# Kernel optimization log

Hardware: AMD Instinct MI355X
Metric: run time of the kernel (lower is better)

Reference implementation:

```python
import jax, jax.numpy as jnp
import numpy as np

B, T, D, H = 512, 512, 128, 64


def _lstm(x, Wih, Whh, b):
    """Single-layer batch-first LSTM, PyTorch gate order (i, f, g, o).
    x: [B, T, Din]; Wih: [4Hc, Din]; Whh: [4Hc, Hc]; b: [4Hc] (= b_ih + b_hh).
    Returns (outputs [B, T, Hc], final_hidden [B, Hc]).
    """
    Hc = Whh.shape[1]
    Bn = x.shape[0]
    # Precompute input projections for all timesteps: [B, T, 4Hc]
    xp = jnp.einsum('bti,gi->btg', x, Wih) + b

    def step(carry, xt):
        h, c = carry
        g = xt + h @ Whh.T                      # [B, 4Hc]
        i = jax.nn.sigmoid(g[:, :Hc])
        f = jax.nn.sigmoid(g[:, Hc:2 * Hc])
        gg = jnp.tanh(g[:, 2 * Hc:3 * Hc])
        o = jax.nn.sigmoid(g[:, 3 * Hc:])
        c = f * c + i * gg
        h = o * jnp.tanh(c)
        return (h, c), h

    init = (jnp.zeros((Bn, Hc), x.dtype), jnp.zeros((Bn, Hc), x.dtype))
    (h_last, _), ys = jax.lax.scan(step, init, jnp.swapaxes(xp, 0, 1))
    return jnp.swapaxes(ys, 0, 1), h_last


def setup_inputs() -> dict:
    key = jax.random.key(0)
    ks = jax.random.split(key, 7)
    se = 1.0 / np.sqrt(H)   # PyTorch LSTM init scale (encoder, hidden=H)
    sd = 1.0 / np.sqrt(D)   # decoder, hidden=D
    return {
        'x': jax.random.normal(ks[0], (B, T, D), jnp.float32),
        'Wih_e': jax.random.uniform(ks[1], (4 * H, D), jnp.float32, -se, se),
        'Whh_e': jax.random.uniform(ks[2], (4 * H, H), jnp.float32, -se, se),
        'b_e': jax.random.uniform(ks[3], (4 * H,), jnp.float32, -se, se),
        'Wih_d': jax.random.uniform(ks[4], (4 * D, H), jnp.float32, -sd, sd),
        'Whh_d': jax.random.uniform(ks[5], (4 * D, D), jnp.float32, -sd, sd),
        'b_d': jax.random.uniform(ks[6], (4 * D,), jnp.float32, -sd, sd),
    }


def reference(x, Wih_e, Whh_e, b_e, Wih_d, Whh_d, b_d):
    # Encoder: take final hidden state [B, H]
    _, h = _lstm(x, Wih_e, Whh_e, b_e)
    # hidden.repeat(T,1,1).permute(1,0,2) -> tile across time: [B, T, H]
    hrep = jnp.broadcast_to(h[:, None, :], (h.shape[0], x.shape[1], h.shape[1]))
    # Decoder: full output sequence [B, T, D]
    reconstructed, _ = _lstm(hrep, Wih_d, Whh_d, b_d)
    return reconstructed
```

## Files before the change

### kernel.cpp

```cpp
#include <hip/hip_runtime.h>

#define TT 512

typedef float f32x2 __attribute__((ext_vector_type(2)));
typedef float f32x4 __attribute__((ext_vector_type(4)));

template<int CTRL>
__device__ __forceinline__ float dpp_mov(float v) {
    return __int_as_float(__builtin_amdgcn_mov_dpp(__float_as_int(v), CTRL, 0xF, 0xF, true));
}
__device__ __forceinline__ float swz_xor4(float v) {
    return __int_as_float(__builtin_amdgcn_ds_swizzle(__float_as_int(v), 0x101F));
}
__device__ __forceinline__ void pk(f32x2& a, f32x2 w, f32x2 v) {
    asm("v_pk_fma_f32 %0, %1, %2, %0" : "+v"(a) : "v"(w), "v"(v));
}

__device__ __forceinline__ float merge8(float* s) {
    s[0] += dpp_mov<0xB1>(s[4]);
    s[1] += dpp_mov<0xB1>(s[5]);
    s[2] += dpp_mov<0xB1>(s[6]);
    s[3] += dpp_mov<0xB1>(s[7]);
    s[0] += dpp_mov<0x4E>(s[2]);
    s[1] += dpp_mov<0x4E>(s[3]);
    return s[0] + swz_xor4(s[1]);
}

__global__ __launch_bounds__(1024, 4)
void dec_kernel(const float* __restrict__ h_enc,
                const float* __restrict__ Wih,
                const float* __restrict__ Whh,
                const float* __restrict__ bias,
                float* __restrict__ out)
{
    const int tid = threadIdx.x;
    const int gg  = tid >> 3;
    const int q   = tid & 7;
    const int q0 = q & 1, q1 = (q >> 1) & 1, q2 = (q >> 2) & 1;
    const int msk2 = (q0 << 1) | q1;
    const int b0  = blockIdx.x * 2;

    __shared__ __align__(16) float he[2][64];
    __shared__ __align__(16) float hb[2][2 * 160];

    if (tid < 128) he[tid >> 6][tid & 63] = h_enc[(size_t)(b0 + (tid >> 6)) * 64 + (tid & 63)];
    if (tid < 256) {
        int r = tid >> 7, j = tid & 127;
        hb[0][r * 160 + j + 4 * (j >> 4)] = 0.f;
    }

    f32x4 w[4][4];
    #pragma unroll
    for (int m = 0; m < 4; ++m) {
        const float* src = Whh + (size_t)((m ^ msk2) * 128 + gg) * 128 + 16 * q;
        #pragma unroll
        for (int c = 0; c < 4; ++c) w[m][c] = *(const f32x4*)(src + 4 * c);
    }

    const int t4own = 2 * q0 + q1;
    const float sA = (t4own == 2) ? 2.f : 1.f;
    const float sC = (t4own == 2) ? -1.f : 0.f;
    const bool writer = (q0 == 0) && (q1 == 0);
    const int rr  = q2;
    const int oA  = q2 * 160;
    const int oB  = (q2 ^ 1) * 160;
    const int kres = 20 * q;
    const int pwj = q2 * 160 + gg + 4 * (gg >> 4);

    __syncthreads();

    float xp;
    {
        const float* heA = he[q2] + 8 * q;
        const float* heB = he[q2 ^ 1] + 8 * q;
        f32x4 hA0 = *(const f32x4*)heA, hA1 = *(const f32x4*)(heA + 4);
        f32x4 hB0 = *(const f32x4*)heB, hB1 = *(const f32x4*)(heB + 4);
        float s[8];
        #pragma unroll
        for (int m = 0; m < 4; ++m) {
            const float* ws = Wih + (size_t)((m ^ msk2) * 128 + gg) * 64 + 8 * q;
            f32x4 w0 = *(const f32x4*)ws, w1 = *(const f32x4*)(ws + 4);
            f32x2 aA = {0.f, 0.f}, aB = {0.f, 0.f};
            pk(aA, w0.lo, hA0.lo); pk(aA, w0.hi, hA0.hi);
            pk(aA, w1.lo, hA1.lo); pk(aA, w1.hi, hA1.hi);
            pk(aB, w0.lo, hB0.lo); pk(aB, w0.hi, hB0.hi);
            pk(aB, w1.lo, hB1.lo); pk(aB, w1.hi, hB1.hi);
            s[2 * m]     = aA.x + aA.y;
            s[2 * m + 1] = aB.x + aB.y;
        }
        xp = merge8(s) + bias[t4own * 128 + gg];
    }

    float c_state = 0.f;
    size_t optr = ((size_t)(b0 + rr) * TT) * 128 + gg;

#define DSTEP(CUR, NXT) {                                                      \
    const float* bAp = (CUR) + oA + kres;                                      \
    const float* bBp = (CUR) + oB + kres;                                      \
    f32x4 ch[4]; f32x2 accA[4], accB[4];                                       \
    _Pragma("unroll") for (int c = 0; c < 4; ++c) ch[c] = *(const f32x4*)(bAp + 4 * c); \
    _Pragma("unroll") for (int m = 0; m < 4; ++m) { f32x2 z2 = {0.f, 0.f};     \
        _Pragma("unroll") for (int c = 0; c < 4; ++c) { pk(z2, w[m][c].lo, ch[c].lo); pk(z2, w[m][c].hi, ch[c].hi); } \
        accA[m] = z2; }                                                        \
    _Pragma("unroll") for (int c = 0; c < 4; ++c) ch[c] = *(const f32x4*)(bBp + 4 * c); \
    _Pragma("unroll") for (int m = 0; m < 4; ++m) { f32x2 z2 = {0.f, 0.f};     \
        _Pragma("unroll") for (int c = 0; c < 4; ++c) { pk(z2, w[m][c].lo, ch[c].lo); pk(z2, w[m][c].hi, ch[c].hi); } \
        accB[m] = z2; }                                                        \
    float s[8];                                                                \
    _Pragma("unroll") for (int m = 0; m < 4; ++m) {                            \
        s[2 * m] = accA[m].x + accA[m].y; s[2 * m + 1] = accB[m].x + accB[m].y; } \
    float z = merge8(s) + xp;                                                  \
    float ez = __expf(-z * sA);                                                \
    float v  = fmaf(__builtin_amdgcn_rcpf(1.0f + ez), sA, sC);                 \
    float vi = dpp_mov<0x00>(v); float vg = dpp_mov<0x55>(v);                  \
    float vf = dpp_mov<0xAA>(v); float vo = dpp_mov<0xFF>(v);                  \
    c_state = fmaf(vf, c_state, vi * vg);                                      \
    float e2 = __expf(-2.f * c_state);                                         \
    float hv = vo * fmaf(__builtin_amdgcn_rcpf(1.f + e2), 2.f, -1.f);          \
    if (writer) { (NXT)[pwj] = hv; out[optr] = hv; }                           \
    optr += 128;                                                               \
    __syncthreads(); }

    #pragma unroll 1
    for (int t = 0; t < TT; t += 2) {
        DSTEP(hb[0], hb[1]);
        DSTEP(hb[1], hb[0]);
    }
#undef DSTEP
}

__global__ __launch_bounds__(512, 2)
void enc_kernel(const float* __restrict__ x,
                const float* __restrict__ Wih,
                const float* __restrict__ Whh,
                const float* __restrict__ bias,
                float* __restrict__ h_out)
{
    const int tid = threadIdx.x;
    const int gg  = tid >> 3;
    const int q   = tid & 7;
    const int q0 = q & 1, q1 = (q >> 1) & 1, q2 = (q >> 2) & 1;
    const int msk2 = (q0 << 1) | q1;
    const int b0  = blockIdx.x * 2;

    __shared__ __align__(16) float xh[2][2 * 224];

    f32x4 w[4][6];
    #pragma unroll
    for (int m = 0; m < 4; ++m) {
        int row = (m ^ msk2) * 64 + gg;
        #pragma unroll
        for (int c = 0; c < 6; ++c) {
            int k0 = 24 * q + 4 * c;
            const float* src = (k0 < 128) ? (Wih + (size_t)row * 128 + k0)
                                          : (Whh + (size_t)row * 64 + (k0 - 128));
            w[m][c] = *(const f32x4*)src;
        }
    }

    const int t4own = 2 * q0 + q1;
    const float sA = (t4own == 2) ? 2.f : 1.f;
    const float sC = (t4own == 2) ? -1.f : 0.f;
    const bool writer = (q0 == 0) && (q1 == 0);
    const int rr  = q2;
    const int oA  = q2 * 224;
    const int oB  = (q2 ^ 1) * 224;
    const int kres = 28 * q;
    const int hj  = 128 + gg;
    const int pwj = q2 * 224 + hj + 4 * (hj / 24);
    const float xpc = bias[t4own * 64 + gg];

    const bool stager = (tid < 64);
    const int sr = (tid >> 5) & 1, sc = tid & 31;
    const int psl = sr * 224 + 4 * sc + 4 * ((4 * sc) / 24);
    const float* xbase = x + ((size_t)(b0 + sr) * TT) * 128 + 4 * sc;

    if (stager) *(f32x4*)(&xh[0][psl]) = *(const f32x4*)xbase;
    if (tid < 128) {
        int r = tid >> 6, j = 128 + (tid & 63);
        xh[0][r * 224 + j + 4 * (j / 24)] = 0.f;
    }

    float c_state = 0.f;
    float h_last = 0.f;
    __syncthreads();

#define ESTEP(CUR, NXT, T) {                                                   \
    f32x4 xnext;                                                               \
    if (stager) { int tl = (T) + 1 < TT ? (T) + 1 : TT - 1;                    \
        xnext = *(const f32x4*)(xbase + (size_t)tl * 128); }                   \
    const float* bAp = (CUR) + oA + kres;                                      \
    const float* bBp = (CUR) + oB + kres;                                      \
    f32x4 ch[6]; f32x2 accA[4], accB[4];                                       \
    _Pragma("unroll") for (int c = 0; c < 6; ++c) ch[c] = *(const f32x4*)(bAp + 4 * c); \
    _Pragma("unroll") for (int m = 0; m < 4; ++m) { f32x2 z2 = {0.f, 0.f};     \
        _Pragma("unroll") for (int c = 0; c < 6; ++c) { pk(z2, w[m][c].lo, ch[c].lo); pk(z2, w[m][c].hi, ch[c].hi); } \
        accA[m] = z2; }                                                        \
    _Pragma("unroll") for (int c = 0; c < 6; ++c) ch[c] = *(const f32x4*)(bBp + 4 * c); \
    _Pragma("unroll") for (int m = 0; m < 4; ++m) { f32x2 z2 = {0.f, 0.f};     \
        _Pragma("unroll") for (int c = 0; c < 6; ++c) { pk(z2, w[m][c].lo, ch[c].lo); pk(z2, w[m][c].hi, ch[c].hi); } \
        accB[m] = z2; }                                                        \
    float s[8];                                                                \
    _Pragma("unroll") for (int m = 0; m < 4; ++m) {                            \
        s[2 * m] = accA[m].x + accA[m].y; s[2 * m + 1] = accB[m].x + accB[m].y; } \
    float z = merge8(s) + xpc;                                                 \
    float ez = __expf(-z * sA);                                                \
    float v  = fmaf(__builtin_amdgcn_rcpf(1.0f + ez), sA, sC);                 \
    float vi = dpp_mov<0x00>(v); float vg = dpp_mov<0x55>(v);                  \
    float vf = dpp_mov<0xAA>(v); float vo = dpp_mov<0xFF>(v);                  \
    c_state = fmaf(vf, c_state, vi * vg);                                      \
    float e2 = __expf(-2.f * c_state);                                         \
    float hv = vo * fmaf(__builtin_amdgcn_rcpf(1.f + e2), 2.f, -1.f);          \
    h_last = hv;                                                               \
    if (writer) (NXT)[pwj] = hv;                                               \
    if (stager) *(f32x4*)((NXT) + psl) = xnext;                                \
    __syncthreads(); }

    #pragma unroll 1
    for (int t = 0; t < TT; t += 2) {
        ESTEP(xh[0], xh[1], t);
        ESTEP(xh[1], xh[0], t + 1);
    }
#undef ESTEP

    if (writer) h_out[(size_t)(b0 + rr) * 64 + gg] = h_last;
}

extern "C" void kernel_launch(void* const* d_in, const int* in_sizes, int n_in,
                              void* d_out, int out_size, void* d_ws, size_t ws_size,
                              hipStream_t stream) {
    const float* x     = (const float*)d_in[0];
    const float* Wih_e = (const float*)d_in[1];
    const float* Whh_e = (const float*)d_in[2];
    const float* b_e   = (const float*)d_in[3];
    const float* Wih_d = (const float*)d_in[4];
    const float* Whh_d = (const float*)d_in[5];
    const float* b_d   = (const float*)d_in[6];
    float* out   = (float*)d_out;
    float* h_enc = (float*)d_ws;

    enc_kernel<<<dim3(256), dim3(512), 0, stream>>>(x, Wih_e, Whh_e, b_e, h_enc);
    dec_kernel<<<dim3(256), dim3(1024), 0, stream>>>(h_enc, Wih_d, Whh_d, b_d, out);
}
```

Baseline: 1.045 ms.

## Split encoder reduction across 16 lanes per gate row with 1024 threads

The encoder kernel now uses 1024 threads per block, with 16 lanes per hidden unit instead of 8. Each lane holds half as many weight registers and does half the FMAs per step, and an extra swizzle stage (merge16) finishes the reduction. The goal is a shorter serial critical path per timestep in the latency-bound recurrence. The price is one more cross-lane reduction step, more threads taking part in each barrier, and a different shared-memory layout without the padding. Both kernels also start their accumulators with v_pk_mul instead of a zero-initialised FMA, and their occupancy hints change to waves_per_eu(4,4).

```diff
diff --git a/kernel.cpp b/kernel.cpp
--- a/kernel.cpp
+++ b/kernel.cpp
@@ -12,8 +12,16 @@
 __device__ __forceinline__ float swz_xor4(float v) {
     return __int_as_float(__builtin_amdgcn_ds_swizzle(__float_as_int(v), 0x101F));
 }
+__device__ __forceinline__ float swz_xor8(float v) {
+    return __int_as_float(__builtin_amdgcn_ds_swizzle(__float_as_int(v), 0x201F));
+}
 __device__ __forceinline__ void pk(f32x2& a, f32x2 w, f32x2 v) {
     asm("v_pk_fma_f32 %0, %1, %2, %0" : "+v"(a) : "v"(w), "v"(v));
+}
+__device__ __forceinline__ f32x2 pkmul(f32x2 w, f32x2 v) {
+    f32x2 a;
+    asm("v_pk_mul_f32 %0, %1, %2" : "=v"(a) : "v"(w), "v"(v));
+    return a;
 }
 
 __device__ __forceinline__ float merge8(float* s) {
@@ -25,8 +33,13 @@
     s[1] += dpp_mov<0x4E>(s[3]);
     return s[0] + swz_xor4(s[1]);
 }
-
-__global__ __launch_bounds__(1024, 4)
+__device__ __forceinline__ float merge16(float* s) {
+    float r = merge8(s);
+    return r + swz_xor8(r);
+}
+
+__global__ __launch_bounds__(1024)
+__attribute__((amdgpu_waves_per_eu(4, 4)))
 void dec_kernel(const float* __restrict__ h_enc,
                 const float* __restrict__ Wih,
                 const float* __restrict__ Whh,
@@ -80,11 +93,10 @@
         for (int m = 0; m < 4; ++m) {
             const float* ws = Wih + (size_t)((m ^ msk2) * 128 + gg) * 64 + 8 * q;
             f32x4 w0 = *(const f32x4*)ws, w1 = *(const f32x4*)(ws + 4);
-            f32x2 aA = {0.f, 0.f}, aB = {0.f, 0.f};
-            pk(aA, w0.lo, hA0.lo); pk(aA, w0.hi, hA0.hi);
-            pk(aA, w1.lo, hA1.lo); pk(aA, w1.hi, hA1.hi);
-            pk(aB, w0.lo, hB0.lo); pk(aB, w0.hi, hB0.hi);
-            pk(aB, w1.lo, hB1.lo); pk(aB, w1.hi, hB1.hi);
+            f32x2 aA = pkmul(w0.lo, hA0.lo);
+            pk(aA, w0.hi, hA0.hi); pk(aA, w1.lo, hA1.lo); pk(aA, w1.hi, hA1.hi);
+            f32x2 aB = pkmul(w0.lo, hB0.lo);
+            pk(aB, w0.hi, hB0.hi); pk(aB, w1.lo, hB1.lo); pk(aB, w1.hi, hB1.hi);
             s[2 * m]     = aA.x + aA.y;
             s[2 * m + 1] = aB.x + aB.y;
         }
@@ -99,12 +111,14 @@
     const float* bBp = (CUR) + oB + kres;                                      \
     f32x4 ch[4]; f32x2 accA[4], accB[4];                                       \
     _Pragma("unroll") for (int c = 0; c < 4; ++c) ch[c] = *(const f32x4*)(bAp + 4 * c); \
-    _Pragma("unroll") for (int m = 0; m < 4; ++m) { f32x2 z2 = {0.f, 0.f};     \
-        _Pragma("unroll") for (int c = 0; c < 4; ++c) { pk(z2, w[m][c].lo, ch[c].lo); pk(z2, w[m][c].hi, ch[c].hi); } \
+    _Pragma("unroll") for (int m = 0; m < 4; ++m) { f32x2 z2 = pkmul(w[m][0].lo, ch[0].lo); \
+        pk(z2, w[m][0].hi, ch[0].hi);                                          \
+        _Pragma("unroll") for (int c = 1; c < 4; ++c) { pk(z2, w[m][c].lo, ch[c].lo); pk(z2, w[m][c].hi, ch[c].hi); } \
         accA[m] = z2; }                                                        \
     _Pragma("unroll") for (int c = 0; c < 4; ++c) ch[c] = *(const f32x4*)(bBp + 4 * c); \
-    _Pragma("unroll") for (int m = 0; m < 4; ++m) { f32x2 z2 = {0.f, 0.f};     \
-        _Pragma("unroll") for (int c = 0; c < 4; ++c) { pk(z2, w[m][c].lo, ch[c].lo); pk(z2, w[m][c].hi, ch[c].hi); } \
+    _Pragma("unroll") for (int m = 0; m < 4; ++m) { f32x2 z2 = pkmul(w[m][0].lo, ch[0].lo); \
+        pk(z2, w[m][0].hi, ch[0].hi);                                          \
+        _Pragma("unroll") for (int c = 1; c < 4; ++c) { pk(z2, w[m][c].lo, ch[c].lo); pk(z2, w[m][c].hi, ch[c].hi); } \
         accB[m] = z2; }                                                        \
     float s[8];                                                                \
     _Pragma("unroll") for (int m = 0; m < 4; ++m) {                            \
@@ -129,7 +143,8 @@
 #undef DSTEP
 }
 
-__global__ __launch_bounds__(512, 2)
+__global__ __launch_bounds__(1024)
+__attribute__((amdgpu_waves_per_eu(4, 4)))
 void enc_kernel(const float* __restrict__ x,
                 const float* __restrict__ Wih,
                 const float* __restrict__ Whh,
@@ -137,21 +152,21 @@
                 float* __restrict__ h_out)
 {
     const int tid = threadIdx.x;
-    const int gg  = tid >> 3;
-    const int q   = tid & 7;
+    const int gg  = tid >> 4;
+    const int q   = tid & 15;
     const int q0 = q & 1, q1 = (q >> 1) & 1, q2 = (q >> 2) & 1;
     const int msk2 = (q0 << 1) | q1;
     const int b0  = blockIdx.x * 2;
 
-    __shared__ __align__(16) float xh[2][2 * 224];
-
-    f32x4 w[4][6];
+    __shared__ __align__(16) float xh[2][2 * 192];
+
+    f32x4 w[4][3];
     #pragma unroll
     for (int m = 0; m < 4; ++m) {
         int row = (m ^ msk2) * 64 + gg;
         #pragma unroll
-        for (int c = 0; c < 6; ++c) {
-            int k0 = 24 * q + 4 * c;
+        for (int c = 0; c < 3; ++c) {
+            int k0 = 12 * q + 4 * c;
             const float* src = (k0 < 128) ? (Wih + (size_t)row * 128 + k0)
                                           : (Whh + (size_t)row * 64 + (k0 - 128));
             w[m][c] = *(const f32x4*)src;
@@ -161,25 +176,20 @@
     const int t4own = 2 * q0 + q1;
     const float sA = (t4own == 2) ? 2.f : 1.f;
     const float sC = (t4own == 2) ? -1.f : 0.f;
-    const bool writer = (q0 == 0) && (q1 == 0);
-    const int rr  = q2;
-    const int oA  = q2 * 224;
-    const int oB  = (q2 ^ 1) * 224;
-    const int kres = 28 * q;
-    const int hj  = 128 + gg;
-    const int pwj = q2 * 224 + hj + 4 * (hj / 24);
+    const bool writer = (q0 == 0) && (q1 == 0) && (((q >> 3) & 1) == 0);
+    const int oA  = q2 * 192;
+    const int oB  = (q2 ^ 1) * 192;
+    const int kres = 12 * q;
+    const int pwj = q2 * 192 + 128 + gg;
     const float xpc = bias[t4own * 64 + gg];
 
     const bool stager = (tid < 64);
     const int sr = (tid >> 5) & 1, sc = tid & 31;
-    const int psl = sr * 224 + 4 * sc + 4 * ((4 * sc) / 24);
+    const int psl = sr * 192 + 4 * sc;
     const float* xbase = x + ((size_t)(b0 + sr) * TT) * 128 + 4 * sc;
 
     if (stager) *(f32x4*)(&xh[0][psl]) = *(const f32x4*)xbase;
-    if (tid < 128) {
-        int r = tid >> 6, j = 128 + (tid & 63);
-        xh[0][r * 224 + j + 4 * (j / 24)] = 0.f;
-    }
+    if (tid < 128) xh[0][(tid >> 6) * 192 + 128 + (tid & 63)] = 0.f;
 
     float c_state = 0.f;
     float h_last = 0.f;
@@ -191,19 +201,23 @@
         xnext = *(const f32x4*)(xbase + (size_t)tl * 128); }                   \
     const float* bAp = (CUR) + oA + kres;                                      \
     const float* bBp = (CUR) + oB + kres;                                      \
-    f32x4 ch[6]; f32x2 accA[4], accB[4];                                       \
-    _Pragma("unroll") for (int c = 0; c < 6; ++c) ch[c] = *(const f32x4*)(bAp + 4 * c); \
-    _Pragma("unroll") for (int m = 0; m < 4; ++m) { f32x2 z2 = {0.f, 0.f};     \
-        _Pragma("unroll") for (int c = 0; c < 6; ++c) { pk(z2, w[m][c].lo, ch[c].lo); pk(z2, w[m][c].hi, ch[c].hi); } \
+    f32x4 ch[3]; f32x2 accA[4], accB[4];                                       \
+    _Pragma("unroll") for (int c = 0; c < 3; ++c) ch[c] = *(const f32x4*)(bAp + 4 * c); \
+    _Pragma("unroll") for (int m = 0; m < 4; ++m) { f32x2 z2 = pkmul(w[m][0].lo, ch[0].lo); \
+        pk(z2, w[m][0].hi, ch[0].hi);                                          \
+        pk(z2, w[m][1].lo, ch[1].lo); pk(z2, w[m][1].hi, ch[1].hi);            \
+        pk(z2, w[m][2].lo, ch[2].lo); pk(z2, w[m][2].hi, ch[2].hi);            \
         accA[m] = z2; }                                                        \
-    _Pragma("unroll") for (int c = 0; c < 6; ++c) ch[c] = *(const f32x4*)(bBp + 4 * c); \
-    _Pragma("unroll") for (int m = 0; m < 4; ++m) { f32x2 z2 = {0.f, 0.f};     \
-        _Pragma("unroll") for (int c = 0; c < 6; ++c) { pk(z2, w[m][c].lo, ch[c].lo); pk(z2, w[m][c].hi, ch[c].hi); } \
+    _Pragma("unroll") for (int c = 0; c < 3; ++c) ch[c] = *(const f32x4*)(bBp + 4 * c); \
+    _Pragma("unroll") for (int m = 0; m < 4; ++m) { f32x2 z2 = pkmul(w[m][0].lo, ch[0].lo); \
+        pk(z2, w[m][0].hi, ch[0].hi);                                          \
+        pk(z2, w[m][1].lo, ch[1].lo); pk(z2, w[m][1].hi, ch[1].hi);            \
+        pk(z2, w[m][2].lo, ch[2].lo); pk(z2, w[m][2].hi, ch[2].hi);            \
         accB[m] = z2; }                                                        \
     float s[8];                                                                \
     _Pragma("unroll") for (int m = 0; m < 4; ++m) {                            \
         s[2 * m] = accA[m].x + accA[m].y; s[2 * m + 1] = accB[m].x + accB[m].y; } \
-    float z = merge8(s) + xpc;                                                 \
+    float z = merge16(s) + xpc;                                                \
     float ez = __expf(-z * sA);                                                \
     float v  = fmaf(__builtin_amdgcn_rcpf(1.0f + ez), sA, sC);                 \
     float vi = dpp_mov<0x00>(v); float vg = dpp_mov<0x55>(v);                  \
@@ -223,7 +237,7 @@
     }
 #undef ESTEP
 
-    if (writer) h_out[(size_t)(b0 + rr) * 64 + gg] = h_last;
+    if (writer) h_out[(size_t)(b0 + q2) * 64 + gg] = h_last;
 }
 
 extern "C" void kernel_launch(void* const* d_in, const int* in_sizes, int n_in,
@@ -239,6 +253,6 @@
     float* out   = (float*)d_out;
     float* h_enc = (float*)d_ws;
 
-    enc_kernel<<<dim3(256), dim3(512), 0, stream>>>(x, Wih_e, Whh_e, b_e, h_enc);
+    enc_kernel<<<dim3(256), dim3(1024), 0, stream>>>(x, Wih_e, Whh_e, b_e, h_enc);
     dec_kernel<<<dim3(256), dim3(1024), 0, stream>>>(h_enc, Wih_d, Whh_d, b_d, out);
 }
```

Measured after the change: 1.095 ms. 4.8% more time.
